# Performance work log

Measured on AMD Instinct MI355X. Metric: run time of the kernel, lower is better.

The kernel has to match this reference:

```python
import jax, jax.numpy as jnp
import numpy as np

B, T, E, M, V = 256, 256, 512, 16, 32000
EPS = 1e-6


def layer_norm(x, g, b):
    m = x.mean(-1, keepdims=True)
    v = x.var(-1, keepdims=True)
    return (x - m) / jnp.sqrt(v + EPS) * g + b


def setup_inputs() -> dict:
    key = jax.random.key(0)
    ks = jax.random.split(key, 12)
    s = 0.02
    return {
        "hidden_state": jax.random.normal(ks[0], (B, 1, E), jnp.float32),
        "output_sequence": jax.random.randint(ks[1], (B, T), 0, V),
        "emb_out": jax.random.normal(ks[2], (V, E), jnp.float32) * s,
        "Wq": jax.random.normal(ks[3], (E, E), jnp.float32) * s,
        "bq": jnp.zeros((E,), jnp.float32),
        "Wk": jax.random.normal(ks[4], (E, E), jnp.float32) * s,
        "bk": jnp.zeros((E,), jnp.float32),
        "Wv": jax.random.normal(ks[5], (E, E), jnp.float32) * s,
        "bv": jnp.zeros((E,), jnp.float32),
        "mover_w": jax.random.normal(ks[6], (M, E), jnp.float32) * s,  # decoder_mover.weight
        "gamma": jnp.ones((E,), jnp.float32),
        "beta": jnp.zeros((E,), jnp.float32),
        "vocab_W": jax.random.normal(ks[7], (E, V), jnp.float32) * s,
        "vocab_b": jnp.zeros((V,), jnp.float32),
    }


def reference(hidden_state, output_sequence, emb_out, Wq, bq, Wk, bk, Wv, bv,
              mover_w, gamma, beta, vocab_W, vocab_b):
    # Embeddings: lookup * sqrt(embed_dim) (annotated-transformer convention)
    x = emb_out[output_sequence] * jnp.sqrt(jnp.float32(E))  # [B, T, E]
    b = x.shape[0]
    # mover = (zeros_like(z)+1) * weight[None]  -> broadcast weight over batch
    mover = jnp.broadcast_to(mover_w[None], (b, M, E))
    # Precompute K/V projections of the constant mover rows once per step inside scan
    scale = 1.0 / jnp.sqrt(jnp.float32(E))

    def step(z, xt):                       # z: [B, E], xt: [B, E]
        z = z + xt
        g = jnp.concatenate([z[:, None, :], mover], axis=1)  # [B, 1+M, E]
        # only row 0 of dg is used -> query only the z token (same math)
        q = z @ Wq + bq                    # [B, E]
        k = g @ Wk + bk                    # [B, 1+M, E]
        v = g @ Wv + bv                    # [B, 1+M, E]
        att = jax.nn.softmax(jnp.einsum('be,bne->bn', q, k) * scale, axis=-1)
        dg0 = jnp.einsum('bn,bne->be', att, v)
        z = layer_norm(z + dg0, gamma, beta)
        return z, None

    z0 = hidden_state[:, 0, :]
    z, _ = jax.lax.scan(step, z0, jnp.swapaxes(x, 0, 1))
    z = z[:, None, :]                      # [B, 1, E]
    y = jax.nn.log_softmax(z @ vocab_W + vocab_b, axis=-1)  # [B, 1, V]
    return (z, y)
```

## Files before the change

kernel.cpp:

```cpp
#include <hip/hip_runtime.h>

#define B_ 256
#define T_ 256
#define E_ 512
#define V_ 32000
#define NMOV 16
#define NT 65
#define NCG 16
#define NBG 16
#define YSTR 1056
#define ZSTR 520

#define SQRTE 22.62741699796952f
#define SCALE 0.04419417382415922f

typedef __attribute__((ext_vector_type(8))) short bf16x8;
typedef __attribute__((ext_vector_type(4))) short bf16x4;
typedef __attribute__((ext_vector_type(4))) float f32x4;
typedef unsigned long long u64;

__device__ __forceinline__ short f2bf(float f) {
  unsigned u = __float_as_uint(f);
  u += 0x7fffu + ((u >> 16) & 1u);
  return (short)(u >> 16);
}
__device__ __forceinline__ float bf2f(short s) {
  return __uint_as_float(((unsigned)(unsigned short)s) << 16);
}

__device__ __forceinline__ float wredsum(float v) {
  int x;
  x = __builtin_amdgcn_update_dpp(0, __float_as_int(v), 0xB1, 0xF, 0xF, true);
  v += __int_as_float(x);
  x = __builtin_amdgcn_update_dpp(0, __float_as_int(v), 0x4E, 0xF, 0xF, true);
  v += __int_as_float(x);
  x = __builtin_amdgcn_update_dpp(0, __float_as_int(v), 0x141, 0xF, 0xF, true);
  v += __int_as_float(x);
  x = __builtin_amdgcn_update_dpp(0, __float_as_int(v), 0x140, 0xF, 0xF, true);
  v += __int_as_float(x);
  x = __builtin_amdgcn_update_dpp(0, __float_as_int(v), 0x142, 0xF, 0xF, true);
  v += __int_as_float(x);
  x = __builtin_amdgcn_update_dpp(0, __float_as_int(v), 0x143, 0xF, 0xF, true);
  v += __int_as_float(x);
  return __int_as_float(__builtin_amdgcn_readlane(__float_as_int(v), 63));
}
__device__ __forceinline__ float rowmax16(float v) {
  int x;
  x = __builtin_amdgcn_update_dpp(0, __float_as_int(v), 0xB1, 0xF, 0xF, true);
  v = fmaxf(v, __int_as_float(x));
  x = __builtin_amdgcn_update_dpp(0, __float_as_int(v), 0x4E, 0xF, 0xF, true);
  v = fmaxf(v, __int_as_float(x));
  x = __builtin_amdgcn_update_dpp(0, __float_as_int(v), 0x141, 0xF, 0xF, true);
  v = fmaxf(v, __int_as_float(x));
  x = __builtin_amdgcn_update_dpp(0, __float_as_int(v), 0x140, 0xF, 0xF, true);
  v = fmaxf(v, __int_as_float(x));
  return v;
}
__device__ __forceinline__ float rowsum16(float v) {
  int x;
  x = __builtin_amdgcn_update_dpp(0, __float_as_int(v), 0xB1, 0xF, 0xF, true);
  v += __int_as_float(x);
  x = __builtin_amdgcn_update_dpp(0, __float_as_int(v), 0x4E, 0xF, 0xF, true);
  v += __int_as_float(x);
  x = __builtin_amdgcn_update_dpp(0, __float_as_int(v), 0x141, 0xF, 0xF, true);
  v += __int_as_float(x);
  x = __builtin_amdgcn_update_dpp(0, __float_as_int(v), 0x140, 0xF, 0xF, true);
  v += __int_as_float(x);
  return v;
}
__device__ __forceinline__ float rdlane(float v, int lane) {
  return __int_as_float(__builtin_amdgcn_readlane(__float_as_int(v), lane));
}

__device__ __forceinline__ bf16x8 aload8v(const short* p) {
  union { u64 u[2]; bf16x8 v; } c;
  c.u[0] = __hip_atomic_load((const u64*)p,       __ATOMIC_RELAXED, __HIP_MEMORY_SCOPE_AGENT);
  c.u[1] = __hip_atomic_load((const u64*)(p + 4), __ATOMIC_RELAXED, __HIP_MEMORY_SCOPE_AGENT);
  return c.v;
}
__device__ __forceinline__ void astore4v(short* p, bf16x4 v) {
  union { bf16x4 v; u64 u; } c; c.v = v;
  __hip_atomic_store((u64*)p, c.u, __ATOMIC_RELAXED, __HIP_MEMORY_SCOPE_AGENT);
}

__global__ void k_movers(const float* __restrict__ Wk, const float* __restrict__ bk,
                         const float* __restrict__ Wv, const float* __restrict__ bv,
                         const float* __restrict__ mover, float* __restrict__ kmvm)
{
  const int m = blockIdx.x & 15;
  const int s = blockIdx.x >> 4;
  const float* W  = s ? Wv : Wk;
  const float* bb = s ? bv : bk;
  const int c = threadIdx.x * 2;
  float a0 = bb[c], a1 = bb[c + 1];
  for (int r = 0; r < E_; ++r) {
    float mv = mover[m * E_ + r];
    float2 wv = *(const float2*)(W + (size_t)r * E_ + c);
    a0 += mv * wv.x; a1 += mv * wv.y;
  }
  kmvm[(s * NMOV + m) * E_ + c]     = a0;
  kmvm[(s * NMOV + m) * E_ + c + 1] = a1;
}

__global__ void k_gemmA(const float* __restrict__ Wq, const float* __restrict__ Wk,
                        float* __restrict__ A)
{
  const int ti = blockIdx.x >> 5, tj = blockIdx.x & 31;
  const int l = threadIdx.x, r16 = l & 15, kq = (l >> 4) * 8;
  f32x4 acc = {0.f, 0.f, 0.f, 0.f};
  for (int ks = 0; ks < 16; ++ks) {
    const float* ap = Wq + (size_t)(ti * 16 + r16) * E_ + ks * 32 + kq;
    const float* bp = Wk + (size_t)(tj * 16 + r16) * E_ + ks * 32 + kq;
    bf16x8 a, b;
    #pragma unroll
    for (int j = 0; j < 8; ++j) { a[j] = f2bf(ap[j]); b[j] = f2bf(bp[j]); }
    acc = __builtin_amdgcn_mfma_f32_16x16x32_bf16(a, b, acc, 0, 0, 0);
  }
  #pragma unroll
  for (int r = 0; r < 4; ++r)
    A[(size_t)(ti * 16 + (l >> 4) * 4 + r) * E_ + tj * 16 + r16] = acc[r];
}

__global__ void k_wqk(const float* __restrict__ Wq, const float* __restrict__ kmvm,
                      float* __restrict__ Wqk)
{
  const int i = blockIdx.x;
  const int l = threadIdx.x, m = l & 15, sl = l >> 4;
  float p = 0.f;
  for (int j = sl * 128; j < sl * 128 + 128; ++j)
    p += Wq[(size_t)i * E_ + j] * kmvm[(size_t)m * E_ + j];
  p += __shfl_xor(p, 16, 64);
  p += __shfl_xor(p, 32, 64);
  if (l < 16) Wqk[i * 16 + m] = p;
}

__global__ void k_cvec(const float* __restrict__ Wq, const float* __restrict__ Wk,
                       const float* __restrict__ bq, const float* __restrict__ bk,
                       float* __restrict__ cvec)
{
  const int i = blockIdx.x * 64 + threadIdx.x;
  float s = 0.f;
  for (int j = 0; j < E_; ++j)
    s += Wq[(size_t)i * E_ + j] * bk[j] + Wk[(size_t)i * E_ + j] * bq[j];
  cvec[i] = s;
}

__global__ void k_lb(const float* __restrict__ bq, const float* __restrict__ bk,
                     const float* __restrict__ kmvm, float* __restrict__ lb)
{
  const int l = threadIdx.x;
  if (l < 16) {
    float s = 0.f;
    for (int j = 0; j < E_; ++j) s += bq[j] * kmvm[(size_t)l * E_ + j];
    lb[l] = s;
  } else if (l == 16) {
    float s = 0.f;
    for (int j = 0; j < E_; ++j) s += bq[j] * bk[j];
    lb[16] = s;
  }
}

__global__ void k_pack(const float* __restrict__ A, const float* __restrict__ Wv,
                       const float* __restrict__ Wqk, short* __restrict__ Wfrag)
{
  const int blk = blockIdx.x;
  const int ct = blk >> 4, ks = blk & 15;
  const int l = threadIdx.x;
  const int c = ct * 16 + (l & 15);
  const int r0 = ks * 32 + (l >> 4) * 8;
  short v[8];
  #pragma unroll
  for (int j = 0; j < 8; ++j) {
    const int r = r0 + j;
    float x;
    if (c < 512)       x = A[(size_t)r * E_ + c];
    else if (c < 1024) x = Wv[(size_t)r * E_ + (c - 512)];
    else               x = Wqk[r * 16 + (c - 1024)];
    v[j] = f2bf(x);
  }
  *(bf16x8*)(Wfrag + ((size_t)blk * 64 + l) * 8) = *(const bf16x8*)v;
}

__global__ __launch_bounds__(512, 2) void k_scan6(
    const float* __restrict__ hidden, const int* __restrict__ seq,
    const float* __restrict__ emb,
    const float* __restrict__ gamma, const float* __restrict__ beta,
    const float* __restrict__ bv,
    const float* __restrict__ kmvm, const float* __restrict__ cvec,
    const float* __restrict__ lb, const short* __restrict__ Wfrag,
    short* __restrict__ Yx, unsigned* __restrict__ flags,
    float* __restrict__ zout)
{
  extern __shared__ char smem[];
  short* wlds    = (short*)smem;
  short* zfs     = (short*)(smem + 81920);
  short* vmfragT = (short*)(smem + 98304);
  float* umov    = (float*)(smem + 114688);
  short* attf    = (short*)(smem + 147968);

  const int tid = threadIdx.x, l = tid & 63, w = tid >> 6;
  const int cg = blockIdx.x >> 4;
  const int bg = blockIdx.x & 15;
  const int ntiles = (cg == 15) ? 5 : 4;
  const int lm = l & 15;

  for (int i = tid; i < 32 * 32; i += 512) {
    const int tile = i >> 5, ln = i & 31;
    const int m0 = (ln >> 4) * 8, c = tile * 16 + (ln & 15);
    short tmp[8];
    #pragma unroll
    for (int j = 0; j < 8; ++j)
      tmp[j] = f2bf(kmvm[NMOV * E_ + (size_t)(m0 + j) * E_ + c]);
    *(bf16x8*)&vmfragT[((size_t)tile * 32 + ln) * 8] = *(const bf16x8*)tmp;
  }
  for (int i = tid; i < 16 * 40; i += 512) attf[i] = 0;
  {
    const bf16x8* src = (const bf16x8*)(Wfrag + (size_t)(cg * 4) * 16 * 64 * 8);
    bf16x8* dst = (bf16x8*)wlds;
    for (int i = tid; i < ntiles * 16 * 64; i += 512) dst[i] = src[i];
  }

  float cw[8], bw[8], gw[8], bb[8];
  *(float4*)&cw[0] = *(const float4*)(cvec  + l * 8);
  *(float4*)&cw[4] = *(const float4*)(cvec  + l * 8 + 4);
  *(float4*)&bw[0] = *(const float4*)(bv    + l * 8);
  *(float4*)&bw[4] = *(const float4*)(bv    + l * 8 + 4);
  *(float4*)&gw[0] = *(const float4*)(gamma + l * 8);
  *(float4*)&gw[4] = *(const float4*)(gamma + l * 8 + 4);
  *(float4*)&bb[0] = *(const float4*)(beta  + l * 8);
  *(float4*)&bb[4] = *(const float4*)(beta  + l * 8 + 4);
  const float lbw  = lb[lm];
  const float lb16 = lb[16];

  const int b0 = bg * 16 + w * 2;
  float zr[2][8];
  #pragma unroll
  for (int bi = 0; bi < 2; ++bi) {
    *(float4*)&zr[bi][0] = *(const float4*)(hidden + (size_t)(b0 + bi) * E_ + l * 8);
    *(float4*)&zr[bi][4] = *(const float4*)(hidden + (size_t)(b0 + bi) * E_ + l * 8 + 4);
  }

  const int sq0 = b0 * T_, sq1 = (b0 + 1) * T_;
  int ian = seq[sq0], ibn = seq[sq1];
  float4 ea0 = *(const float4*)(emb + (size_t)ian * E_ + l * 8);
  float4 ea1 = *(const float4*)(emb + (size_t)ian * E_ + l * 8 + 4);
  float4 eb0 = *(const float4*)(emb + (size_t)ibn * E_ + l * 8);
  float4 eb1 = *(const float4*)(emb + (size_t)ibn * E_ + l * 8 + 4);
  ian = seq[sq0 + 1]; ibn = seq[sq1 + 1];

  unsigned* const flagline = flags + bg * 32;
  __syncthreads();

  #pragma unroll 1
  for (int t = 0; t < T_; ++t) {
    const int p = t & 1;
    {
      float xa[8] = {ea0.x, ea0.y, ea0.z, ea0.w, ea1.x, ea1.y, ea1.z, ea1.w};
      float xb[8] = {eb0.x, eb0.y, eb0.z, eb0.w, eb1.x, eb1.y, eb1.z, eb1.w};
      short ta[8], tb[8];
      #pragma unroll
      for (int j = 0; j < 8; ++j) {
        zr[0][j] += xa[j] * SQRTE; ta[j] = f2bf(zr[0][j]);
        zr[1][j] += xb[j] * SQRTE; tb[j] = f2bf(zr[1][j]);
      }
      const int ks = l >> 2;
      const int ua = ((l & 3) << 4) | (w * 2);
      const int ub = ua | 1;
      *(bf16x8*)&zfs[((ks << 6) + (ua ^ (ks & 7))) * 8] = *(const bf16x8*)ta;
      *(bf16x8*)&zfs[((ks << 6) + (ub ^ (ks & 7))) * 8] = *(const bf16x8*)tb;
    }
    if (t + 1 < T_) {
      ea0 = *(const float4*)(emb + (size_t)ian * E_ + l * 8);
      ea1 = *(const float4*)(emb + (size_t)ian * E_ + l * 8 + 4);
      eb0 = *(const float4*)(emb + (size_t)ibn * E_ + l * 8);
      eb1 = *(const float4*)(emb + (size_t)ibn * E_ + l * 8 + 4);
      if (t + 2 < T_) { ian = seq[sq0 + t + 2]; ibn = seq[sq1 + t + 2]; }
    }
    __syncthreads();

    if (w < ntiles) {
      f32x4 acc = {0.f, 0.f, 0.f, 0.f};
      #pragma unroll
      for (int ks = 0; ks < 16; ++ks) {
        bf16x8 wf = *(const bf16x8*)&wlds[((w * 16 + ks) * 64 + l) * 8];
        bf16x8 zb = *(const bf16x8*)&zfs[((ks << 6) + (l ^ (ks & 7))) * 8];
        acc = __builtin_amdgcn_mfma_f32_16x16x32_bf16(wf, zb, acc, 0, 0, 0);
      }
      const int gt = cg * 4 + w;
      bf16x4 o;
      #pragma unroll
      for (int r = 0; r < 4; ++r) o[r] = f2bf(acc[r]);
      astore4v(Yx + (((size_t)(p * NBG + bg) * 16) + lm) * YSTR
                  + gt * 16 + ((l >> 4) << 2), o);
      asm volatile("s_waitcnt vmcnt(0)" ::: "memory");
    }
    __syncthreads();

    if (tid == 0)
      __hip_atomic_store(&flagline[cg], (unsigned)(t + 1),
                         __ATOMIC_RELAXED, __HIP_MEMORY_SCOPE_AGENT);
    {
      const unsigned rnd = (unsigned)(t + 1);
      for (;;) {
        unsigned f = __hip_atomic_load(&flagline[lm], __ATOMIC_RELAXED,
                                       __HIP_MEMORY_SCOPE_AGENT);
        if (__all(lm == cg || f >= rnd)) break;
        __builtin_amdgcn_s_sleep(1);
      }
      asm volatile("" ::: "memory");
    }

    const short* Yb  = Yx + ((size_t)(p * NBG + bg) * 16) * YSTR;
    const short* Yr0 = Yb + (size_t)(w * 2) * YSTR;
    const short* Yr1 = Yb + (size_t)(w * 2 + 1) * YSTR;
    bf16x8 wv0 = aload8v(Yr0 + l * 8),       wv1 = aload8v(Yr1 + l * 8);
    bf16x8 vv0 = aload8v(Yr0 + 512 + l * 8), vv1 = aload8v(Yr1 + 512 + l * 8);
    const short* Yrh = (l < 32) ? Yr0 : Yr1;
    short mlr = (short)__hip_atomic_load((const short*)(Yrh + 1024 + lm),
                                         __ATOMIC_RELAXED, __HIP_MEMORY_SCOPE_AGENT);

    float p0 = 0.f, p1 = 0.f;
    #pragma unroll
    for (int j = 0; j < 8; ++j) {
      p0 += (bf2f(wv0[j]) + cw[j]) * zr[0][j];
      p1 += (bf2f(wv1[j]) + cw[j]) * zr[1][j];
    }
    const float dl0 = (wredsum(p0) + lb16) * SCALE;
    const float dl1 = (wredsum(p1) + lb16) * SCALE;

    const float dl   = (l < 32) ? dl0 : dl1;
    const float lgt  = (bf2f(mlr) + lbw) * SCALE;
    const float mx   = fmaxf(rowmax16(lgt), dl);
    const float e    = __expf(lgt - mx);
    const float a0v  = __expf(dl - mx);
    const float den  = rowsum16(e) + a0v;
    if ((l & 16) == 0)
      attf[(w * 2 + (l >> 5)) * 40 + lm] = f2bf(e);

    const float a00 = rdlane(a0v, 0),  a01 = rdlane(a0v, 32);
    const float rd0 = __fdividef(1.f, rdlane(den, 0));
    const float rd1 = __fdividef(1.f, rdlane(den, 32));

    __syncthreads();

    #pragma unroll
    for (int tt = 0; tt < 4; ++tt) {
      const int tile = w * 4 + tt;
      bf16x8 af = {0, 0, 0, 0, 0, 0, 0, 0};
      if (l < 32) af = *(const bf16x8*)&vmfragT[((size_t)tile * 32 + l) * 8];
      bf16x8 bf = *(const bf16x8*)&attf[lm * 40 + (l >> 4) * 8];
      f32x4 z4 = {0.f, 0.f, 0.f, 0.f};
      z4 = __builtin_amdgcn_mfma_f32_16x16x32_bf16(af, bf, z4, 0, 0, 0);
      *(f32x4*)&umov[(size_t)lm * 520 + tile * 16 + ((l >> 4) << 2)] = z4;
    }
    __syncthreads();

    {
      float um0[8], um1[8], u0[8], u1[8];
      *(float4*)&um0[0] = *(const float4*)&umov[(size_t)(w * 2) * 520 + l * 8];
      *(float4*)&um0[4] = *(const float4*)&umov[(size_t)(w * 2) * 520 + l * 8 + 4];
      *(float4*)&um1[0] = *(const float4*)&umov[(size_t)(w * 2 + 1) * 520 + l * 8];
      *(float4*)&um1[4] = *(const float4*)&umov[(size_t)(w * 2 + 1) * 520 + l * 8 + 4];
      #pragma unroll
      for (int j = 0; j < 8; ++j) {
        u0[j] = zr[0][j] + (a00 * (bf2f(vv0[j]) + bw[j]) + um0[j]) * rd0;
        u1[j] = zr[1][j] + (a01 * (bf2f(vv1[j]) + bw[j]) + um1[j]) * rd1;
      }
      float s10 = 0.f, s20 = 0.f, s11 = 0.f, s21 = 0.f;
      #pragma unroll
      for (int j = 0; j < 8; ++j) {
        s10 += u0[j]; s20 += u0[j] * u0[j];
        s11 += u1[j]; s21 += u1[j] * u1[j];
      }
      s10 = wredsum(s10); s20 = wredsum(s20);
      s11 = wredsum(s11); s21 = wredsum(s21);
      const float mean0 = s10 * (1.f / 512.f);
      const float mean1 = s11 * (1.f / 512.f);
      const float rstd0 = rsqrtf(s20 * (1.f / 512.f) - mean0 * mean0 + 1e-6f);
      const float rstd1 = rsqrtf(s21 * (1.f / 512.f) - mean1 * mean1 + 1e-6f);
      #pragma unroll
      for (int j = 0; j < 8; ++j) {
        zr[0][j] = (u0[j] - mean0) * rstd0 * gw[j] + bb[j];
        zr[1][j] = (u1[j] - mean1) * rstd1 * gw[j] + bb[j];
      }
    }
  }

  if (cg == 0) {
    #pragma unroll
    for (int bi = 0; bi < 2; ++bi) {
      *(float4*)(zout + (size_t)(b0 + bi) * E_ + l * 8)     = *(float4*)&zr[bi][0];
      *(float4*)(zout + (size_t)(b0 + bi) * E_ + l * 8 + 4) = *(float4*)&zr[bi][4];
    }
  }
}

#define K2_SMEM (128 * ZSTR * 2)

__global__ __launch_bounds__(512, 2) void k_logits(
    const float* __restrict__ z, const float* __restrict__ W,
    const float* __restrict__ bia, float* __restrict__ out)
{
  extern __shared__ short zl[];
  const int tid = threadIdx.x;
  const int btile = blockIdx.x & 1;
  const int vt = blockIdx.x >> 1;
  for (int i = tid; i < 128 * 128; i += 512) {
    int row = i >> 7, c4 = (i & 127) << 2;
    float4 zv = *(const float4*)(z + (size_t)(btile * 128 + row) * E_ + c4);
    short* d = zl + row * ZSTR + c4;
    d[0] = f2bf(zv.x); d[1] = f2bf(zv.y); d[2] = f2bf(zv.z); d[3] = f2bf(zv.w);
  }
  __syncthreads();
  const int lane = tid & 63, w = tid >> 6;
  const int vc = vt * 128 + w * 16 + (lane & 15);
  const int kq = (lane >> 4) * 8;
  f32x4 acc[8];
  #pragma unroll
  for (int rt = 0; rt < 8; ++rt) acc[rt] = (f32x4){0.f, 0.f, 0.f, 0.f};
  for (int ks = 0; ks < 16; ++ks) {
    bf16x8 bf;
    #pragma unroll
    for (int j = 0; j < 8; ++j)
      bf[j] = f2bf(W[(size_t)(ks * 32 + kq + j) * V_ + vc]);
    #pragma unroll
    for (int rt = 0; rt < 8; ++rt) {
      bf16x8 a = *(const bf16x8*)&zl[(rt * 16 + (lane & 15)) * ZSTR + ks * 32 + kq];
      acc[rt] = __builtin_amdgcn_mfma_f32_16x16x32_bf16(a, bf, acc[rt], 0, 0, 0);
    }
  }
  const float bbv = bia[vc];
  #pragma unroll
  for (int rt = 0; rt < 8; ++rt)
    #pragma unroll
    for (int r = 0; r < 4; ++r)
      out[(size_t)(btile * 128 + rt * 16 + (lane >> 4) * 4 + r) * V_ + vc] = acc[rt][r] + bbv;
}

__global__ void k_logsoftmax(float* __restrict__ y)
{
  float* L = y + (size_t)blockIdx.x * V_;
  float m = -3.402823466e+38f, s = 0.f;
  for (int i = threadIdx.x; i < V_; i += 256) {
    float l = L[i];
    if (l > m) { s = s * __expf(m - l) + 1.f; m = l; }
    else       { s += __expf(l - m); }
  }
  #pragma unroll
  for (int k = 1; k < 64; k <<= 1) {
    float m2 = __shfl_xor(m, k, 64);
    float s2 = __shfl_xor(s, k, 64);
    float M = fmaxf(m, m2);
    s = s * __expf(m - M) + s2 * __expf(m2 - M);
    m = M;
  }
  __shared__ float ms[4], ss[4];
  if ((threadIdx.x & 63) == 0) { ms[threadIdx.x >> 6] = m; ss[threadIdx.x >> 6] = s; }
  __syncthreads();
  float M = fmaxf(fmaxf(ms[0], ms[1]), fmaxf(ms[2], ms[3]));
  float S = ss[0] * __expf(ms[0] - M) + ss[1] * __expf(ms[1] - M) +
            ss[2] * __expf(ms[2] - M) + ss[3] * __expf(ms[3] - M);
  const float lse = M + logf(S);
  for (int i = threadIdx.x; i < V_; i += 256) L[i] -= lse;
}

#define SCAN_SMEM 149248

extern "C" void kernel_launch(void* const* d_in, const int* in_sizes, int n_in,
                              void* d_out, int out_size, void* d_ws, size_t ws_size,
                              hipStream_t stream) {
  const float* hidden = (const float*)d_in[0];
  const int*   seq    = (const int*)  d_in[1];
  const float* emb    = (const float*)d_in[2];
  const float* Wq     = (const float*)d_in[3];
  const float* bq     = (const float*)d_in[4];
  const float* Wk     = (const float*)d_in[5];
  const float* bk     = (const float*)d_in[6];
  const float* Wv     = (const float*)d_in[7];
  const float* bv     = (const float*)d_in[8];
  const float* mover  = (const float*)d_in[9];
  const float* gamma  = (const float*)d_in[10];
  const float* beta   = (const float*)d_in[11];
  const float* vocabW = (const float*)d_in[12];
  const float* vocabB = (const float*)d_in[13];

  float* zoutp = (float*)d_out;
  float* yout  = zoutp + (size_t)B_ * E_;

  short*    Wfrag = (short*)yout;
  float*    A     = yout + 266240;
  float*    Wqk   = A + 262144;
  float*    cvec  = Wqk + 8192;
  float*    lbp   = cvec + 512;
  float*    kmvmS = lbp + 32;
  short*    Yx    = (short*)(kmvmS + 16384);
  unsigned* flags = (unsigned*)(Yx + 540672);

  hipMemsetAsync(flags, 0, 16 * 32 * 4, stream);
  hipLaunchKernelGGL(k_movers, dim3(32), dim3(256), 0, stream, Wk, bk, Wv, bv, mover, kmvmS);
  hipLaunchKernelGGL(k_gemmA,  dim3(1024), dim3(64), 0, stream, Wq, Wk, A);
  hipLaunchKernelGGL(k_wqk,    dim3(512), dim3(64), 0, stream, Wq, kmvmS, Wqk);
  hipLaunchKernelGGL(k_cvec,   dim3(8), dim3(64), 0, stream, Wq, Wk, bq, bk, cvec);
  hipLaunchKernelGGL(k_lb,     dim3(1), dim3(64), 0, stream, bq, bk, kmvmS, lbp);
  hipLaunchKernelGGL(k_pack,   dim3(NT * 16), dim3(64), 0, stream, A, Wv, Wqk, Wfrag);

  hipFuncSetAttribute((const void*)k_scan6, hipFuncAttributeMaxDynamicSharedMemorySize, SCAN_SMEM);
  void* args[] = {(void*)&hidden, (void*)&seq, (void*)&emb,
                  (void*)&gamma, (void*)&beta, (void*)&bv,
                  (void*)&kmvmS, (void*)&cvec, (void*)&lbp, (void*)&Wfrag,
                  (void*)&Yx, (void*)&flags, (void*)&zoutp};
  hipLaunchCooperativeKernel((const void*)k_scan6, dim3(NCG * NBG), dim3(512),
                             args, SCAN_SMEM, stream);

  hipFuncSetAttribute((const void*)k_logits, hipFuncAttributeMaxDynamicSharedMemorySize, K2_SMEM);
  hipLaunchKernelGGL(k_logits, dim3(500), dim3(512), K2_SMEM, stream, zoutp, vocabW, vocabB, yout);
  hipLaunchKernelGGL(k_logsoftmax, dim3(256), dim3(256), 0, stream, yout);
}
```

Before: 1.298 ms.

## Process two batch groups per block to overlap flag waits with compute

The scan kernel now launches half as many blocks, and each block handles two batch groups (A and B). The GEMM phase for both groups runs across all 8 waves. The elementwise and layer-norm phase for group A runs while group B's cross-block flags are still arriving, and the next step's embedding add and bf16 packing are fused into the end of that phase. The mover output buffer changes from fp32 to bf16 to make room for a second z buffer. The intent is to hide inter-block sync latency and use MFMA units more fully, at the cost of fewer blocks, more registers and extra bf16 rounding of the mover term.

```diff
diff --git a/kernel.cpp b/kernel.cpp
--- a/kernel.cpp
+++ b/kernel.cpp
@@ -181,7 +181,106 @@
   *(bf16x8*)(Wfrag + ((size_t)blk * 64 + l) * 8) = *(const bf16x8*)v;
 }
 
-__global__ __launch_bounds__(512, 2) void k_scan6(
+__device__ __forceinline__ void phase_b(
+    int p, int bg, int l, int w,
+    const short* __restrict__ Yx, short* attf, short* umov,
+    const short* vmfragT, short* zfs_s,
+    float (&zr)[2][8],
+    const float* cw, const float* bw, const float* gw, const float* bbv,
+    float lbw, float lb16,
+    const float* xa, const float* xb, bool addx)
+{
+  const int lm = l & 15;
+  const short* Yb  = Yx + ((size_t)(p * NBG + bg) * 16) * YSTR;
+  const short* Yr0 = Yb + (size_t)(w * 2) * YSTR;
+  const short* Yr1 = Yb + (size_t)(w * 2 + 1) * YSTR;
+  bf16x8 wv0 = aload8v(Yr0 + l * 8),       wv1 = aload8v(Yr1 + l * 8);
+  bf16x8 vv0 = aload8v(Yr0 + 512 + l * 8), vv1 = aload8v(Yr1 + 512 + l * 8);
+  const short* Yrh = (l < 32) ? Yr0 : Yr1;
+  short mlr = (short)__hip_atomic_load((const short*)(Yrh + 1024 + lm),
+                                       __ATOMIC_RELAXED, __HIP_MEMORY_SCOPE_AGENT);
+
+  float p0 = 0.f, p1 = 0.f;
+  #pragma unroll
+  for (int j = 0; j < 8; ++j) {
+    p0 += (bf2f(wv0[j]) + cw[j]) * zr[0][j];
+    p1 += (bf2f(wv1[j]) + cw[j]) * zr[1][j];
+  }
+  const float dl0 = (wredsum(p0) + lb16) * SCALE;
+  const float dl1 = (wredsum(p1) + lb16) * SCALE;
+
+  const float dl   = (l < 32) ? dl0 : dl1;
+  const float lgt  = (bf2f(mlr) + lbw) * SCALE;
+  const float mx   = fmaxf(rowmax16(lgt), dl);
+  const float e    = __expf(lgt - mx);
+  const float a0v  = __expf(dl - mx);
+  const float den  = rowsum16(e) + a0v;
+  if ((l & 16) == 0)
+    attf[(w * 2 + (l >> 5)) * 40 + lm] = f2bf(e);
+
+  const float a00 = rdlane(a0v, 0),  a01 = rdlane(a0v, 32);
+  const float rd0 = __fdividef(1.f, rdlane(den, 0));
+  const float rd1 = __fdividef(1.f, rdlane(den, 32));
+
+  __syncthreads();
+
+  #pragma unroll
+  for (int tt = 0; tt < 4; ++tt) {
+    const int tile = w * 4 + tt;
+    bf16x8 af = {0, 0, 0, 0, 0, 0, 0, 0};
+    if (l < 32) af = *(const bf16x8*)&vmfragT[((size_t)tile * 32 + l) * 8];
+    bf16x8 bf = *(const bf16x8*)&attf[lm * 40 + (l >> 4) * 8];
+    f32x4 z4 = {0.f, 0.f, 0.f, 0.f};
+    z4 = __builtin_amdgcn_mfma_f32_16x16x32_bf16(af, bf, z4, 0, 0, 0);
+    bf16x4 o4;
+    #pragma unroll
+    for (int r = 0; r < 4; ++r) o4[r] = f2bf(z4[r]);
+    *(bf16x4*)&umov[(size_t)lm * 528 + tile * 16 + ((l >> 4) << 2)] = o4;
+  }
+  __syncthreads();
+
+  {
+    bf16x8 um0 = *(const bf16x8*)&umov[(size_t)(w * 2) * 528 + l * 8];
+    bf16x8 um1 = *(const bf16x8*)&umov[(size_t)(w * 2 + 1) * 528 + l * 8];
+    float u0[8], u1[8];
+    #pragma unroll
+    for (int j = 0; j < 8; ++j) {
+      u0[j] = zr[0][j] + (a00 * (bf2f(vv0[j]) + bw[j]) + bf2f(um0[j])) * rd0;
+      u1[j] = zr[1][j] + (a01 * (bf2f(vv1[j]) + bw[j]) + bf2f(um1[j])) * rd1;
+    }
+    float s10 = 0.f, s20 = 0.f, s11 = 0.f, s21 = 0.f;
+    #pragma unroll
+    for (int j = 0; j < 8; ++j) {
+      s10 += u0[j]; s20 += u0[j] * u0[j];
+      s11 += u1[j]; s21 += u1[j] * u1[j];
+    }
+    s10 = wredsum(s10); s20 = wredsum(s20);
+    s11 = wredsum(s11); s21 = wredsum(s21);
+    const float mean0 = s10 * (1.f / 512.f);
+    const float mean1 = s11 * (1.f / 512.f);
+    const float rstd0 = rsqrtf(s20 * (1.f / 512.f) - mean0 * mean0 + 1e-6f);
+    const float rstd1 = rsqrtf(s21 * (1.f / 512.f) - mean1 * mean1 + 1e-6f);
+
+    short ta[8], tb[8];
+    #pragma unroll
+    for (int j = 0; j < 8; ++j) {
+      float z0 = (u0[j] - mean0) * rstd0 * gw[j] + bbv[j];
+      float z1 = (u1[j] - mean1) * rstd1 * gw[j] + bbv[j];
+      if (addx) { z0 += xa[j] * SQRTE; z1 += xb[j] * SQRTE; }
+      zr[0][j] = z0; zr[1][j] = z1;
+      ta[j] = f2bf(z0); tb[j] = f2bf(z1);
+    }
+    if (addx) {
+      const int ks = l >> 2;
+      const int ua = ((l & 3) << 4) | (w * 2);
+      const int ub = ua | 1;
+      *(bf16x8*)&zfs_s[((ks << 6) + (ua ^ (ks & 7))) * 8] = *(const bf16x8*)ta;
+      *(bf16x8*)&zfs_s[((ks << 6) + (ub ^ (ks & 7))) * 8] = *(const bf16x8*)tb;
+    }
+  }
+}
+
+__global__ __launch_bounds__(512, 2) void k_scan7(
     const float* __restrict__ hidden, const int* __restrict__ seq,
     const float* __restrict__ emb,
     const float* __restrict__ gamma, const float* __restrict__ beta,
@@ -194,13 +293,14 @@
   extern __shared__ char smem[];
   short* wlds    = (short*)smem;
   short* zfs     = (short*)(smem + 81920);
-  short* vmfragT = (short*)(smem + 98304);
-  float* umov    = (float*)(smem + 114688);
+  short* vmfragT = (short*)(smem + 114688);
+  short* umov    = (short*)(smem + 131072);
   short* attf    = (short*)(smem + 147968);
 
   const int tid = threadIdx.x, l = tid & 63, w = tid >> 6;
-  const int cg = blockIdx.x >> 4;
-  const int bg = blockIdx.x & 15;
+  const int cg  = blockIdx.x >> 3;
+  const int bgp = blockIdx.x & 7;
+  const int bgA = bgp, bgB = bgp + 8;
   const int ntiles = (cg == 15) ? 5 : 4;
   const int lm = l & 15;
 
@@ -220,177 +320,156 @@
     for (int i = tid; i < ntiles * 16 * 64; i += 512) dst[i] = src[i];
   }
 
-  float cw[8], bw[8], gw[8], bb[8];
-  *(float4*)&cw[0] = *(const float4*)(cvec  + l * 8);
-  *(float4*)&cw[4] = *(const float4*)(cvec  + l * 8 + 4);
-  *(float4*)&bw[0] = *(const float4*)(bv    + l * 8);
-  *(float4*)&bw[4] = *(const float4*)(bv    + l * 8 + 4);
-  *(float4*)&gw[0] = *(const float4*)(gamma + l * 8);
-  *(float4*)&gw[4] = *(const float4*)(gamma + l * 8 + 4);
-  *(float4*)&bb[0] = *(const float4*)(beta  + l * 8);
-  *(float4*)&bb[4] = *(const float4*)(beta  + l * 8 + 4);
+  float cw[8], bw[8], gw[8], bbv[8];
+  *(float4*)&cw[0]  = *(const float4*)(cvec  + l * 8);
+  *(float4*)&cw[4]  = *(const float4*)(cvec  + l * 8 + 4);
+  *(float4*)&bw[0]  = *(const float4*)(bv    + l * 8);
+  *(float4*)&bw[4]  = *(const float4*)(bv    + l * 8 + 4);
+  *(float4*)&gw[0]  = *(const float4*)(gamma + l * 8);
+  *(float4*)&gw[4]  = *(const float4*)(gamma + l * 8 + 4);
+  *(float4*)&bbv[0] = *(const float4*)(beta  + l * 8);
+  *(float4*)&bbv[4] = *(const float4*)(beta  + l * 8 + 4);
   const float lbw  = lb[lm];
   const float lb16 = lb[16];
 
-  const int b0 = bg * 16 + w * 2;
-  float zr[2][8];
+  const int b0A = bgA * 16 + w * 2;
+  const int b0B = bgB * 16 + w * 2;
+  float zrA[2][8], zrB[2][8];
   #pragma unroll
   for (int bi = 0; bi < 2; ++bi) {
-    *(float4*)&zr[bi][0] = *(const float4*)(hidden + (size_t)(b0 + bi) * E_ + l * 8);
-    *(float4*)&zr[bi][4] = *(const float4*)(hidden + (size_t)(b0 + bi) * E_ + l * 8 + 4);
-  }
-
-  const int sq0 = b0 * T_, sq1 = (b0 + 1) * T_;
-  int ian = seq[sq0], ibn = seq[sq1];
-  float4 ea0 = *(const float4*)(emb + (size_t)ian * E_ + l * 8);
-  float4 ea1 = *(const float4*)(emb + (size_t)ian * E_ + l * 8 + 4);
-  float4 eb0 = *(const float4*)(emb + (size_t)ibn * E_ + l * 8);
-  float4 eb1 = *(const float4*)(emb + (size_t)ibn * E_ + l * 8 + 4);
-  ian = seq[sq0 + 1]; ibn = seq[sq1 + 1];
-
-  unsigned* const flagline = flags + bg * 32;
+    *(float4*)&zrA[bi][0] = *(const float4*)(hidden + (size_t)(b0A + bi) * E_ + l * 8);
+    *(float4*)&zrA[bi][4] = *(const float4*)(hidden + (size_t)(b0A + bi) * E_ + l * 8 + 4);
+    *(float4*)&zrB[bi][0] = *(const float4*)(hidden + (size_t)(b0B + bi) * E_ + l * 8);
+    *(float4*)&zrB[bi][4] = *(const float4*)(hidden + (size_t)(b0B + bi) * E_ + l * 8 + 4);
+  }
+
+  int sqb[4]; sqb[0] = b0A * T_; sqb[1] = sqb[0] + T_;
+              sqb[2] = b0B * T_; sqb[3] = sqb[2] + T_;
+  int ix[4];
+  float4 exL[4], exH[4];
+  #pragma unroll
+  for (int k = 0; k < 4; ++k) ix[k] = seq[sqb[k]];
+  #pragma unroll
+  for (int k = 0; k < 4; ++k) {
+    exL[k] = *(const float4*)(emb + (size_t)ix[k] * E_ + l * 8);
+    exH[k] = *(const float4*)(emb + (size_t)ix[k] * E_ + l * 8 + 4);
+  }
+  {
+    short t0[8], t1[8], t2[8], t3[8];
+    float x0[8] = {exL[0].x, exL[0].y, exL[0].z, exL[0].w, exH[0].x, exH[0].y, exH[0].z, exH[0].w};
+    float x1[8] = {exL[1].x, exL[1].y, exL[1].z, exL[1].w, exH[1].x, exH[1].y, exH[1].z, exH[1].w};
+    float x2[8] = {exL[2].x, exL[2].y, exL[2].z, exL[2].w, exH[2].x, exH[2].y, exH[2].z, exH[2].w};
+    float x3[8] = {exL[3].x, exL[3].y, exL[3].z, exL[3].w, exH[3].x, exH[3].y, exH[3].z, exH[3].w};
+    #pragma unroll
+    for (int j = 0; j < 8; ++j) {
+      zrA[0][j] += x0[j] * SQRTE; t0[j] = f2bf(zrA[0][j]);
+      zrA[1][j] += x1[j] * SQRTE; t1[j] = f2bf(zrA[1][j]);
+      zrB[0][j] += x2[j] * SQRTE; t2[j] = f2bf(zrB[0][j]);
+      zrB[1][j] += x3[j] * SQRTE; t3[j] = f2bf(zrB[1][j]);
+    }
+    const int ks = l >> 2;
+    const int ua = ((l & 3) << 4) | (w * 2);
+    const int ub = ua | 1;
+    *(bf16x8*)&zfs[((ks << 6) + (ua ^ (ks & 7))) * 8]        = *(const bf16x8*)t0;
+    *(bf16x8*)&zfs[((ks << 6) + (ub ^ (ks & 7))) * 8]        = *(const bf16x8*)t1;
+    *(bf16x8*)&zfs[8192 + ((ks << 6) + (ua ^ (ks & 7))) * 8] = *(const bf16x8*)t2;
+    *(bf16x8*)&zfs[8192 + ((ks << 6) + (ub ^ (ks & 7))) * 8] = *(const bf16x8*)t3;
+  }
+  #pragma unroll
+  for (int k = 0; k < 4; ++k) ix[k] = seq[sqb[k] + 1];
+
+  unsigned* const flA = flags + bgA * 32;
+  unsigned* const flB = flags + bgB * 32;
   __syncthreads();
 
   #pragma unroll 1
   for (int t = 0; t < T_; ++t) {
     const int p = t & 1;
+    const unsigned rnd = (unsigned)(t + 1);
+    const bool addx = (t + 1 < T_);
+
+    if (addx) {
+      #pragma unroll
+      for (int k = 0; k < 4; ++k) {
+        exL[k] = *(const float4*)(emb + (size_t)ix[k] * E_ + l * 8);
+        exH[k] = *(const float4*)(emb + (size_t)ix[k] * E_ + l * 8 + 4);
+      }
+      if (t + 2 < T_) {
+        #pragma unroll
+        for (int k = 0; k < 4; ++k) ix[k] = seq[sqb[k] + t + 2];
+      }
+    }
+
     {
-      float xa[8] = {ea0.x, ea0.y, ea0.z, ea0.w, ea1.x, ea1.y, ea1.z, ea1.w};
-      float xb[8] = {eb0.x, eb0.y, eb0.z, eb0.w, eb1.x, eb1.y, eb1.z, eb1.w};
-      short ta[8], tb[8];
-      #pragma unroll
-      for (int j = 0; j < 8; ++j) {
-        zr[0][j] += xa[j] * SQRTE; ta[j] = f2bf(zr[0][j]);
-        zr[1][j] += xb[j] * SQRTE; tb[j] = f2bf(zr[1][j]);
+      const int slot = w >> 2;
+      const int wl = w & 3;
+      const int bgS = slot ? bgB : bgA;
+      const short* zfs_s = zfs + slot * 8192;
+      for (int lt = wl; lt < ntiles; lt += 4) {
+        f32x4 acc = {0.f, 0.f, 0.f, 0.f};
+        #pragma unroll
+        for (int ks = 0; ks < 16; ++ks) {
+          bf16x8 wf = *(const bf16x8*)&wlds[((lt * 16 + ks) * 64 + l) * 8];
+          bf16x8 zb = *(const bf16x8*)&zfs_s[((ks << 6) + (l ^ (ks & 7))) * 8];
+          acc = __builtin_amdgcn_mfma_f32_16x16x32_bf16(wf, zb, acc, 0, 0, 0);
+        }
+        const int gt = cg * 4 + lt;
+        bf16x4 o;
+        #pragma unroll
+        for (int r = 0; r < 4; ++r) o[r] = f2bf(acc[r]);
+        astore4v(Yx + (((size_t)(p * NBG + bgS) * 16) + lm) * YSTR
+                    + gt * 16 + ((l >> 4) << 2), o);
       }
-      const int ks = l >> 2;
-      const int ua = ((l & 3) << 4) | (w * 2);
-      const int ub = ua | 1;
-      *(bf16x8*)&zfs[((ks << 6) + (ua ^ (ks & 7))) * 8] = *(const bf16x8*)ta;
-      *(bf16x8*)&zfs[((ks << 6) + (ub ^ (ks & 7))) * 8] = *(const bf16x8*)tb;
-    }
-    if (t + 1 < T_) {
-      ea0 = *(const float4*)(emb + (size_t)ian * E_ + l * 8);
-      ea1 = *(const float4*)(emb + (size_t)ian * E_ + l * 8 + 4);
-      eb0 = *(const float4*)(emb + (size_t)ibn * E_ + l * 8);
-      eb1 = *(const float4*)(emb + (size_t)ibn * E_ + l * 8 + 4);
-      if (t + 2 < T_) { ian = seq[sq0 + t + 2]; ibn = seq[sq1 + t + 2]; }
+      asm volatile("s_waitcnt vmcnt(0)" ::: "memory");
     }
     __syncthreads();
 
-    if (w < ntiles) {
-      f32x4 acc = {0.f, 0.f, 0.f, 0.f};
-      #pragma unroll
-      for (int ks = 0; ks < 16; ++ks) {
-        bf16x8 wf = *(const bf16x8*)&wlds[((w * 16 + ks) * 64 + l) * 8];
-        bf16x8 zb = *(const bf16x8*)&zfs[((ks << 6) + (l ^ (ks & 7))) * 8];
-        acc = __builtin_amdgcn_mfma_f32_16x16x32_bf16(wf, zb, acc, 0, 0, 0);
-      }
-      const int gt = cg * 4 + w;
-      bf16x4 o;
-      #pragma unroll
-      for (int r = 0; r < 4; ++r) o[r] = f2bf(acc[r]);
-      astore4v(Yx + (((size_t)(p * NBG + bg) * 16) + lm) * YSTR
-                  + gt * 16 + ((l >> 4) << 2), o);
-      asm volatile("s_waitcnt vmcnt(0)" ::: "memory");
-    }
-    __syncthreads();
-
-    if (tid == 0)
-      __hip_atomic_store(&flagline[cg], (unsigned)(t + 1),
-                         __ATOMIC_RELAXED, __HIP_MEMORY_SCOPE_AGENT);
+    if (tid == 0) {
+      __hip_atomic_store(&flA[cg], rnd, __ATOMIC_RELAXED, __HIP_MEMORY_SCOPE_AGENT);
+      __hip_atomic_store(&flB[cg], rnd, __ATOMIC_RELAXED, __HIP_MEMORY_SCOPE_AGENT);
+    }
+
+    for (;;) {
+      unsigned f = __hip_atomic_load(&flA[lm], __ATOMIC_RELAXED, __HIP_MEMORY_SCOPE_AGENT);
+      if (__all(lm == cg || f >= rnd)) break;
+      __builtin_amdgcn_s_sleep(1);
+    }
+    asm volatile("" ::: "memory");
+
+    unsigned fB = __hip_atomic_load(&flB[lm], __ATOMIC_RELAXED, __HIP_MEMORY_SCOPE_AGENT);
+
     {
-      const unsigned rnd = (unsigned)(t + 1);
+      float xa[8] = {exL[0].x, exL[0].y, exL[0].z, exL[0].w, exH[0].x, exH[0].y, exH[0].z, exH[0].w};
+      float xb[8] = {exL[1].x, exL[1].y, exL[1].z, exL[1].w, exH[1].x, exH[1].y, exH[1].z, exH[1].w};
+      phase_b(p, bgA, l, w, Yx, attf, umov, vmfragT, zfs, zrA,
+              cw, bw, gw, bbv, lbw, lb16, xa, xb, addx);
+    }
+
+    if (!__all(lm == cg || fB >= rnd)) {
       for (;;) {
-        unsigned f = __hip_atomic_load(&flagline[lm], __ATOMIC_RELAXED,
-                                       __HIP_MEMORY_SCOPE_AGENT);
+        unsigned f = __hip_atomic_load(&flB[lm], __ATOMIC_RELAXED, __HIP_MEMORY_SCOPE_AGENT);
         if (__all(lm == cg || f >= rnd)) break;
         __builtin_amdgcn_s_sleep(1);
       }
-      asm volatile("" ::: "memory");
-    }
-
-    const short* Yb  = Yx + ((size_t)(p * NBG + bg) * 16) * YSTR;
-    const short* Yr0 = Yb + (size_t)(w * 2) * YSTR;
-    const short* Yr1 = Yb + (size_t)(w * 2 + 1) * YSTR;
-    bf16x8 wv0 = aload8v(Yr0 + l * 8),       wv1 = aload8v(Yr1 + l * 8);
-    bf16x8 vv0 = aload8v(Yr0 + 512 + l * 8), vv1 = aload8v(Yr1 + 512 + l * 8);
-    const short* Yrh = (l < 32) ? Yr0 : Yr1;
-    short mlr = (short)__hip_atomic_load((const short*)(Yrh + 1024 + lm),
-                                         __ATOMIC_RELAXED, __HIP_MEMORY_SCOPE_AGENT);
-
-    float p0 = 0.f, p1 = 0.f;
-    #pragma unroll
-    for (int j = 0; j < 8; ++j) {
-      p0 += (bf2f(wv0[j]) + cw[j]) * zr[0][j];
-      p1 += (bf2f(wv1[j]) + cw[j]) * zr[1][j];
-    }
-    const float dl0 = (wredsum(p0) + lb16) * SCALE;
-    const float dl1 = (wredsum(p1) + lb16) * SCALE;
-
-    const float dl   = (l < 32) ? dl0 : dl1;
-    const float lgt  = (bf2f(mlr) + lbw) * SCALE;
-    const float mx   = fmaxf(rowmax16(lgt), dl);
-    const float e    = __expf(lgt - mx);
-    const float a0v  = __expf(dl - mx);
-    const float den  = rowsum16(e) + a0v;
-    if ((l & 16) == 0)
-      attf[(w * 2 + (l >> 5)) * 40 + lm] = f2bf(e);
-
-    const float a00 = rdlane(a0v, 0),  a01 = rdlane(a0v, 32);
-    const float rd0 = __fdividef(1.f, rdlane(den, 0));
-    const float rd1 = __fdividef(1.f, rdlane(den, 32));
-
+    }
+    asm volatile("" ::: "memory");
+
+    {
+      float xa[8] = {exL[2].x, exL[2].y, exL[2].z, exL[2].w, exH[2].x, exH[2].y, exH[2].z, exH[2].w};
+      float xb[8] = {exL[3].x, exL[3].y, exL[3].z, exL[3].w, exH[3].x, exH[3].y, exH[3].z, exH[3].w};
+      phase_b(p, bgB, l, w, Yx, attf, umov, vmfragT, zfs + 8192, zrB,
+              cw, bw, gw, bbv, lbw, lb16, xa, xb, addx);
+    }
     __syncthreads();
-
-    #pragma unroll
-    for (int tt = 0; tt < 4; ++tt) {
-      const int tile = w * 4 + tt;
-      bf16x8 af = {0, 0, 0, 0, 0, 0, 0, 0};
-      if (l < 32) af = *(const bf16x8*)&vmfragT[((size_t)tile * 32 + l) * 8];
-      bf16x8 bf = *(const bf16x8*)&attf[lm * 40 + (l >> 4) * 8];
-      f32x4 z4 = {0.f, 0.f, 0.f, 0.f};
-      z4 = __builtin_amdgcn_mfma_f32_16x16x32_bf16(af, bf, z4, 0, 0, 0);
-      *(f32x4*)&umov[(size_t)lm * 520 + tile * 16 + ((l >> 4) << 2)] = z4;
-    }
-    __syncthreads();
-
-    {
-      float um0[8], um1[8], u0[8], u1[8];
-      *(float4*)&um0[0] = *(const float4*)&umov[(size_t)(w * 2) * 520 + l * 8];
-      *(float4*)&um0[4] = *(const float4*)&umov[(size_t)(w * 2) * 520 + l * 8 + 4];
-      *(float4*)&um1[0] = *(const float4*)&umov[(size_t)(w * 2 + 1) * 520 + l * 8];
-      *(float4*)&um1[4] = *(const float4*)&umov[(size_t)(w * 2 + 1) * 520 + l * 8 + 4];
-      #pragma unroll
-      for (int j = 0; j < 8; ++j) {
-        u0[j] = zr[0][j] + (a00 * (bf2f(vv0[j]) + bw[j]) + um0[j]) * rd0;
-        u1[j] = zr[1][j] + (a01 * (bf2f(vv1[j]) + bw[j]) + um1[j]) * rd1;
-      }
-      float s10 = 0.f, s20 = 0.f, s11 = 0.f, s21 = 0.f;
-      #pragma unroll
-      for (int j = 0; j < 8; ++j) {
-        s10 += u0[j]; s20 += u0[j] * u0[j];
-        s11 += u1[j]; s21 += u1[j] * u1[j];
-      }
-      s10 = wredsum(s10); s20 = wredsum(s20);
-      s11 = wredsum(s11); s21 = wredsum(s21);
-      const float mean0 = s10 * (1.f / 512.f);
-      const float mean1 = s11 * (1.f / 512.f);
-      const float rstd0 = rsqrtf(s20 * (1.f / 512.f) - mean0 * mean0 + 1e-6f);
-      const float rstd1 = rsqrtf(s21 * (1.f / 512.f) - mean1 * mean1 + 1e-6f);
-      #pragma unroll
-      for (int j = 0; j < 8; ++j) {
-        zr[0][j] = (u0[j] - mean0) * rstd0 * gw[j] + bb[j];
-        zr[1][j] = (u1[j] - mean1) * rstd1 * gw[j] + bb[j];
-      }
-    }
   }
 
   if (cg == 0) {
     #pragma unroll
     for (int bi = 0; bi < 2; ++bi) {
-      *(float4*)(zout + (size_t)(b0 + bi) * E_ + l * 8)     = *(float4*)&zr[bi][0];
-      *(float4*)(zout + (size_t)(b0 + bi) * E_ + l * 8 + 4) = *(float4*)&zr[bi][4];
+      *(float4*)(zout + (size_t)(b0A + bi) * E_ + l * 8)     = *(float4*)&zrA[bi][0];
+      *(float4*)(zout + (size_t)(b0A + bi) * E_ + l * 8 + 4) = *(float4*)&zrA[bi][4];
+      *(float4*)(zout + (size_t)(b0B + bi) * E_ + l * 8)     = *(float4*)&zrB[bi][0];
+      *(float4*)(zout + (size_t)(b0B + bi) * E_ + l * 8 + 4) = *(float4*)&zrB[bi][4];
     }
   }
 }
@@ -504,12 +583,12 @@
   hipLaunchKernelGGL(k_lb,     dim3(1), dim3(64), 0, stream, bq, bk, kmvmS, lbp);
   hipLaunchKernelGGL(k_pack,   dim3(NT * 16), dim3(64), 0, stream, A, Wv, Wqk, Wfrag);
 
-  hipFuncSetAttribute((const void*)k_scan6, hipFuncAttributeMaxDynamicSharedMemorySize, SCAN_SMEM);
+  hipFuncSetAttribute((const void*)k_scan7, hipFuncAttributeMaxDynamicSharedMemorySize, SCAN_SMEM);
   void* args[] = {(void*)&hidden, (void*)&seq, (void*)&emb,
                   (void*)&gamma, (void*)&beta, (void*)&bv,
                   (void*)&kmvmS, (void*)&cvec, (void*)&lbp, (void*)&Wfrag,
                   (void*)&Yx, (void*)&flags, (void*)&zoutp};
-  hipLaunchCooperativeKernel((const void*)k_scan6, dim3(NCG * NBG), dim3(512),
+  hipLaunchCooperativeKernel((const void*)k_scan7, dim3(NCG * 8), dim3(512),
                              args, SCAN_SMEM, stream);
 
   hipFuncSetAttribute((const void*)k_logits, hipFuncAttributeMaxDynamicSharedMemorySize, K2_SMEM);
```

Measured after the change: 2.160 ms. 66.4% more time.
